# Performance work log

Measured on AMD Instinct MI355X. Metric: run time of the kernel, lower is better.

The kernel has to match this reference:

```python
import jax, jax.numpy as jnp
import numpy as np

N = 50000        # nodes
F_IN = 128       # input features
HID = 128        # hidden_size
H = 4            # heads
C = HID // H     # per-head channels (32)
E_RAND = 800000  # random edges; + N self loops -> E = 850000
NEG_SLOPE = 0.2  # PyG GATConv default leaky_relu slope


def setup_inputs() -> dict:
    key = jax.random.key(0)
    ks = jax.random.split(key, 12)
    x = jax.random.normal(ks[0], (N, F_IN), jnp.float32)
    src_r = jax.random.randint(ks[1], (E_RAND,), 0, N)
    dst_r = jax.random.randint(ks[2], (E_RAND,), 0, N)
    loops = jnp.arange(N)
    src = jnp.concatenate([src_r, loops]).astype(jnp.int32)
    dst = jnp.concatenate([dst_r, loops]).astype(jnp.int32)

    def glorot(k, shape):
        fan_in, fan_out = shape[0], shape[-1]
        lim = np.sqrt(6.0 / (fan_in + fan_out)).astype(np.float32)
        return jax.random.uniform(k, shape, jnp.float32, -lim, lim)

    return {
        "x": x, "src": src, "dst": dst,
        "W0": glorot(ks[3], (F_IN, HID)),
        "a_src0": glorot(ks[4], (H, C)),
        "a_dst0": glorot(ks[5], (H, C)),
        "b0": jnp.zeros((HID,), jnp.float32),
        "W1": glorot(ks[6], (HID, HID)),
        "a_src1": glorot(ks[7], (H, C)),
        "a_dst1": glorot(ks[8], (H, C)),
        "b1": jnp.zeros((HID,), jnp.float32),
    }


def gat_layer(x, W, a_src, a_dst, b, src, dst):
    # linear projection -> [N, H, C]
    xp = (x @ W).reshape(-1, H, C)
    # per-node attention logits [N, H]
    al_src = jnp.einsum("nhc,hc->nh", xp, a_src)
    al_dst = jnp.einsum("nhc,hc->nh", xp, a_dst)
    # edge logits [E, H]
    e = jax.nn.leaky_relu(al_src[src] + al_dst[dst], NEG_SLOPE)
    # scatter softmax over incoming edges of each destination node
    m = jax.ops.segment_max(e, dst, num_segments=N)
    p = jnp.exp(e - m[dst])
    s = jax.ops.segment_sum(p, dst, num_segments=N)
    alpha = p / (s[dst] + 1e-16)
    # weighted message aggregation: [E, H, C] scatter-add -> [N, H, C]
    out = jax.ops.segment_sum(xp[src] * alpha[:, :, None], dst, num_segments=N)
    return out.reshape(-1, H * C) + b  # concat heads + bias


def reference(x, src, dst, W0, a_src0, a_dst0, b0, W1, a_src1, a_dst1, b1):
    h = jax.nn.relu(gat_layer(x, W0, a_src0, a_dst0, b0, src, dst))
    h = jax.nn.relu(gat_layer(h, W1, a_src1, a_dst1, b1, src, dst))
    return h
```

## Files before the change

### kernel.cpp

```cpp
#include <hip/hip_runtime.h>
#include <math.h>

#define NEG_SLOPE 0.2f
#define BCAP 4096
#define TILE 8192

using half8 = __attribute__((ext_vector_type(8))) _Float16;
using f32x4 = __attribute__((ext_vector_type(4))) float;

__device__ __forceinline__ float leaky(float x) { return x > 0.f ? x : NEG_SLOPE * x; }

__device__ __forceinline__ float wsum64(float v) {
#pragma unroll
  for (int off = 32; off; off >>= 1) v += __shfl_xor(v, off);
  return v;
}

__device__ __forceinline__ unsigned short f2h(float f) {
  union { _Float16 h; unsigned short u; } x;
  x.h = (_Float16)f;
  return x.u;
}
__device__ __forceinline__ float h2f(unsigned short u) {
  union { unsigned short u; _Float16 h; } x;
  x.u = u;
  return (float)x.h;
}

__device__ __forceinline__ void acc8h(float* a, float p, uint4 rv) {
  union { uint4 v; _Float16 h[8]; } u;
  u.v = rv;
#pragma unroll
  for (int j = 0; j < 8; ++j) a[j] = fmaf(p, (float)u.h[j], a[j]);
}

__device__ __forceinline__ float getp(float p0, float p1, float p2, float p3,
                                      int h, int t) {
  float b0 = __shfl(p0, t), b1 = __shfl(p1, t);
  float b2 = __shfl(p2, t), b3 = __shfl(p3, t);
  float lo = (h & 1) ? b1 : b0;
  float hi = (h & 1) ? b3 : b2;
  return (h & 2) ? hi : lo;
}

#define PA 136
#define PW 40
template <bool AHALF>
__device__ void gemm_body(
    const void* __restrict__ Av, const unsigned short* __restrict__ Wt,
    const float* __restrict__ a_src, const float* __restrict__ a_dst,
    unsigned short* __restrict__ xph, float* __restrict__ als,
    float* __restrict__ ald, int nrows, int blk) {
  __shared__ unsigned short Ah[64 * PA];
  __shared__ unsigned short Al[AHALF ? 64 : 64 * PA];
  __shared__ unsigned short Wh[128 * PW];
  int t = threadIdx.x;
  int row0 = blk * 64;

  if constexpr (!AHALF) {
    const float4* A4 = (const float4*)Av;
#pragma unroll
    for (int p = 0; p < 8; ++p) {
      int idx = t + p * 256;
      int row = idx >> 5, k4 = idx & 31;
      int gr = row0 + row;
      float4 v = make_float4(0.f, 0.f, 0.f, 0.f);
      if (gr < nrows) v = A4[(size_t)gr * 32 + k4];
      ushort4 hi, lo;
      hi.x = f2h(v.x); lo.x = f2h(v.x - h2f(hi.x));
      hi.y = f2h(v.y); lo.y = f2h(v.y - h2f(hi.y));
      hi.z = f2h(v.z); lo.z = f2h(v.z - h2f(hi.z));
      hi.w = f2h(v.w); lo.w = f2h(v.w - h2f(hi.w));
      *(ushort4*)&Ah[row * PA + k4 * 4] = hi;
      *(ushort4*)&Al[row * PA + k4 * 4] = lo;
    }
  } else {
    const uint4* A4 = (const uint4*)Av;
#pragma unroll
    for (int p = 0; p < 4; ++p) {
      int idx = t + p * 256;
      int row = idx >> 4, k8 = idx & 15;
      int gr = row0 + row;
      uint4 v = make_uint4(0u, 0u, 0u, 0u);
      if (gr < nrows) v = A4[(size_t)gr * 16 + k8];
      *(uint4*)&Ah[row * PA + k8 * 8] = v;
    }
  }

  int lane = t & 63, wv = t >> 6;
  int wr = wv >> 1, wc = wv & 1;
  int ml = lane & 15, q = lane >> 4;
  f32x4 acc[2][4] = {};

  for (int kb = 0; kb < 4; ++kb) {
    __syncthreads();
    int k0 = kb * 32;
#pragma unroll
    for (int p = 0; p < 8; ++p) {
      int idx = t + p * 256;
      int n = idx >> 4, kp = idx & 15;
      *(unsigned*)&Wh[n * PW + kp * 2] =
          *(const unsigned*)(Wt + (size_t)n * 128 + k0 + kp * 2);
    }
    __syncthreads();
    int kf = k0 + q * 8;
    half8 a_h0 = *(const half8*)&Ah[(wr * 32 + ml) * PA + kf];
    half8 a_h1 = *(const half8*)&Ah[(wr * 32 + 16 + ml) * PA + kf];
    half8 a_l0, a_l1;
    if constexpr (!AHALF) {
      a_l0 = *(const half8*)&Al[(wr * 32 + ml) * PA + kf];
      a_l1 = *(const half8*)&Al[(wr * 32 + 16 + ml) * PA + kf];
    }
#pragma unroll
    for (int ct = 0; ct < 4; ++ct) {
      int nb = (wc * 64 + ct * 16 + ml) * PW + q * 8;
      half8 b = *(const half8*)&Wh[nb];
      acc[0][ct] = __builtin_amdgcn_mfma_f32_16x16x32_f16(a_h0, b, acc[0][ct], 0, 0, 0);
      if constexpr (!AHALF)
        acc[0][ct] = __builtin_amdgcn_mfma_f32_16x16x32_f16(a_l0, b, acc[0][ct], 0, 0, 0);
      acc[1][ct] = __builtin_amdgcn_mfma_f32_16x16x32_f16(a_h1, b, acc[1][ct], 0, 0, 0);
      if constexpr (!AHALF)
        acc[1][ct] = __builtin_amdgcn_mfma_f32_16x16x32_f16(a_l1, b, acc[1][ct], 0, 0, 0);
    }
  }

  float asr[4], adr[4];
#pragma unroll
  for (int ct = 0; ct < 4; ++ct) {
    int col = (wc * 2 + (ct >> 1)) * 32 + (ct & 1) * 16 + ml;
    asr[ct] = a_src[col];
    adr[ct] = a_dst[col];
  }

#pragma unroll
  for (int rt = 0; rt < 2; ++rt) {
#pragma unroll
    for (int r = 0; r < 4; ++r) {
      int gr = row0 + wr * 32 + rt * 16 + q * 4 + r;
      bool valid = gr < nrows;
      if (valid) {
#pragma unroll
        for (int ct = 0; ct < 4; ++ct) {
          int gc = wc * 64 + ct * 16 + ml;
          xph[(size_t)gr * 128 + gc] = f2h(acc[rt][ct][r]);
        }
      }
      float p0 = acc[rt][0][r] * asr[0] + acc[rt][1][r] * asr[1];
      float p1 = acc[rt][2][r] * asr[2] + acc[rt][3][r] * asr[3];
      float d0 = acc[rt][0][r] * adr[0] + acc[rt][1][r] * adr[1];
      float d1 = acc[rt][2][r] * adr[2] + acc[rt][3][r] * adr[3];
#pragma unroll
      for (int off = 1; off <= 8; off <<= 1) {
        p0 += __shfl_xor(p0, off); p1 += __shfl_xor(p1, off);
        d0 += __shfl_xor(d0, off); d1 += __shfl_xor(d1, off);
      }
      if (ml == 0 && valid) {
        als[(size_t)gr * 4 + wc * 2] = p0;
        als[(size_t)gr * 4 + wc * 2 + 1] = p1;
        ald[(size_t)gr * 4 + wc * 2] = d0;
        ald[(size_t)gr * 4 + wc * 2 + 1] = d1;
      }
    }
  }
}

__global__ __launch_bounds__(256) void k_hist_wsplit(
    const int* __restrict__ dst, int* __restrict__ blkhist, int E, int nb, int nblk,
    const float* __restrict__ W0, const float* __restrict__ W1,
    unsigned short* __restrict__ Wt0, unsigned short* __restrict__ Wt1) {
  __shared__ int h[512];
  if (blockIdx.x < 128) {
    int i = blockIdx.x * 256 + threadIdx.x;
    int j = i & 16383;
    int k = j >> 7, n = j & 127;
    const float* W = (i < 16384) ? W0 : W1;
    unsigned short hv = f2h(W[j]);
    if (i < 16384) Wt0[n * 128 + k] = hv;
    else Wt1[n * 128 + k] = hv;
    return;
  }
  int blk = blockIdx.x - 128;
  for (int i = threadIdx.x; i < nb; i += 256) h[i] = 0;
  __syncthreads();
  int t0 = blk * TILE;
  int end = t0 + TILE < E ? t0 + TILE : E;
  for (int i = t0 + threadIdx.x; i < end; i += 256) atomicAdd(&h[dst[i] >> 7], 1);
  __syncthreads();
  for (int i = threadIdx.x; i < nb; i += 256) blkhist[(size_t)i * nblk + blk] = h[i];
}

__global__ __launch_bounds__(256) void k_bofs(int* __restrict__ blkhist,
                                              int* __restrict__ btot, int nblk) {
  __shared__ int sd[256];
  int b = blockIdx.x, t = threadIdx.x;
  int v = (t < nblk) ? blkhist[(size_t)b * nblk + t] : 0;
  sd[t] = v;
  __syncthreads();
  for (int off = 1; off < 256; off <<= 1) {
    int add = (t >= off) ? sd[t - off] : 0;
    __syncthreads();
    sd[t] += add;
    __syncthreads();
  }
  if (t < nblk) blkhist[(size_t)b * nblk + t] = sd[t] - v;
  if (t == 255) btot[b] = sd[255];
}

__global__ __launch_bounds__(256, 3) void k_scatter2_gemm(
    const int* __restrict__ src, const int* __restrict__ dst,
    const int* __restrict__ blkhist, const int* __restrict__ btot,
    int* __restrict__ bstore, int E, int nb, int nblk,
    const float* __restrict__ A, const unsigned short* __restrict__ Wt,
    const float* __restrict__ a_src, const float* __restrict__ a_dst,
    unsigned short* __restrict__ xph, float* __restrict__ als,
    float* __restrict__ ald, int nrows) {
  if ((int)blockIdx.x >= nblk) {
    gemm_body<false>(A, Wt, a_src, a_dst, xph, als, ald, nrows, blockIdx.x - nblk);
    return;
  }
  __shared__ int sd[256];
  __shared__ int bb[512];
  __shared__ int cur[512];
  int t = threadIdx.x, blk = blockIdx.x;
  int v0 = (2 * t < nb) ? btot[2 * t] : 0;
  int v1 = (2 * t + 1 < nb) ? btot[2 * t + 1] : 0;
  int s = v0 + v1;
  sd[t] = s;
  __syncthreads();
  for (int off = 1; off < 256; off <<= 1) {
    int add = (t >= off) ? sd[t - off] : 0;
    __syncthreads();
    sd[t] += add;
    __syncthreads();
  }
  int run = sd[t] - s;
  if (2 * t < nb) bb[2 * t] = run;
  if (2 * t + 1 < nb) bb[2 * t + 1] = run + v0;
  __syncthreads();
  for (int i = t; i < nb; i += 256)
    cur[i] = bb[i] + blkhist[(size_t)i * nblk + blk];
  __syncthreads();
  int t0 = blk * TILE;
  int end = t0 + TILE < E ? t0 + TILE : E;
  for (int i = t0 + t; i < end; i += 256) {
    int d = dst[i];
    int pos = atomicAdd(&cur[d >> 7], 1);
    bstore[pos] = ((d & 127) << 16) | src[i];
  }
}

__global__ __launch_bounds__(256) void k_build(
    const int* __restrict__ bstore, const int* __restrict__ btot,
    int* __restrict__ ssrc, int* __restrict__ deg, int* __restrict__ rstart, int N) {
  __shared__ int ls[BCAP];
  __shared__ unsigned char lloc[BCAP];
  __shared__ int lout[BCAP];
  __shared__ int hist[128];
  __shared__ int sc[128];
  __shared__ int lcur[128];
  __shared__ int red[256];
  int b = blockIdx.x;
  int t = threadIdx.x;
  int pacc = 0;
  for (int j = t; j < b; j += 256) pacc += btot[j];
  red[t] = pacc;
  __syncthreads();
  for (int off = 128; off; off >>= 1) {
    if (t < off) red[t] += red[t + off];
    __syncthreads();
  }
  int base = red[0];
  int cnt = btot[b];
  if (cnt > BCAP) cnt = BCAP;
  int nlo = b << 7;
  if (t < 128) { hist[t] = 0; lcur[t] = 0; }
  __syncthreads();
  for (int i = t; i < cnt; i += 256) {
    int e = bstore[base + i];
    int loc = e >> 16;
    ls[i] = e & 0xffff;
    lloc[i] = (unsigned char)loc;
    atomicAdd(&hist[loc], 1);
  }
  __syncthreads();
  int hv = (t < 128) ? hist[t] : 0;
  if (t < 128) sc[t] = hv;
  __syncthreads();
  for (int off = 1; off < 128; off <<= 1) {
    int add = (t < 128 && t >= off) ? sc[t - off] : 0;
    __syncthreads();
    if (t < 128) sc[t] += add;
    __syncthreads();
  }
  int lstart = (t < 128) ? sc[t] - hv : 0;
  if (t < 128) sc[t] = lstart;
  if (t < 128 && nlo + t < N) {
    deg[nlo + t] = hv;
    rstart[nlo + t] = base + lstart;
  }
  __syncthreads();
  for (int i = t; i < cnt; i += 256) {
    int loc = lloc[i];
    int slot = sc[loc] + atomicAdd(&lcur[loc], 1);
    lout[slot] = ls[i];
  }
  __syncthreads();
  for (int i = t; i < cnt; i += 256) ssrc[base + i] = lout[i];
}

__global__ __launch_bounds__(256, 3) void k_gemm2(
    const unsigned short* __restrict__ A, const unsigned short* __restrict__ Wt,
    const float* __restrict__ a_src, const float* __restrict__ a_dst,
    unsigned short* __restrict__ xph, float* __restrict__ als,
    float* __restrict__ ald, int nrows) {
  gemm_body<true>(A, Wt, a_src, a_dst, xph, als, ald, nrows, blockIdx.x);
}

template <bool HOUT>
__global__ __launch_bounds__(256) void k_aggregate(
    const unsigned short* __restrict__ xph, const float* __restrict__ als,
    const float* __restrict__ ald, const int* __restrict__ rstart,
    const int* __restrict__ deg, const int* __restrict__ ssrc,
    const float* __restrict__ bias, void* __restrict__ outv, int N) {
  __shared__ float pbuf[4][128 * 4];
  __shared__ int snbuf[4][128];
  int wv = threadIdx.x >> 6;
  int lane = threadIdx.x & 63;
  int n = (blockIdx.x * blockDim.x + threadIdx.x) >> 6;
  if (n >= N) return;
  int start = rstart[n];
  int d = deg[n];
  float4 adv = *(const float4*)(ald + (size_t)n * 4);

  int cg = lane & 15;
  int es = lane >> 4;
  int c0 = cg * 8;
  int h = cg >> 2;
  float a[8] = {0.f, 0.f, 0.f, 0.f, 0.f, 0.f, 0.f, 0.f};
  float s0 = 0.f, s1 = 0.f, s2 = 0.f, s3 = 0.f;
  const uint4* xp4 = (const uint4*)xph;

  if (d <= 64) {
    bool valid = lane < d;
    int sn = ssrc[start + (valid ? lane : 0)];
    float4 av = *(const float4*)(als + (size_t)sn * 4);
    int sA = __shfl(sn, es);
    int sB = __shfl(sn, es + 4);
    int sC = __shfl(sn, es + 8);
    int sD = __shfl(sn, es + 12);
    uint4 r0 = xp4[(size_t)sA * 16 + cg];
    uint4 r1 = xp4[(size_t)sB * 16 + cg];
    uint4 r2 = xp4[(size_t)sC * 16 + cg];
    uint4 r3 = xp4[(size_t)sD * 16 + cg];
    float p0 = valid ? __expf(leaky(av.x + adv.x)) : 0.f;
    float p1 = valid ? __expf(leaky(av.y + adv.y)) : 0.f;
    float p2 = valid ? __expf(leaky(av.z + adv.z)) : 0.f;
    float p3 = valid ? __expf(leaky(av.w + adv.w)) : 0.f;
    acc8h(a, getp(p0, p1, p2, p3, h, es), r0);
    if (d > 4)  acc8h(a, getp(p0, p1, p2, p3, h, es + 4), r1);
    if (d > 8)  acc8h(a, getp(p0, p1, p2, p3, h, es + 8), r2);
    if (d > 12) acc8h(a, getp(p0, p1, p2, p3, h, es + 12), r3);
    for (int tb = 16; tb < d; tb += 4) {
      int t = tb + es;
      int st = __shfl(sn, t);
      uint4 rv = xp4[(size_t)st * 16 + cg];
      acc8h(a, getp(p0, p1, p2, p3, h, t), rv);
    }
    s0 = wsum64(p0); s1 = wsum64(p1); s2 = wsum64(p2); s3 = wsum64(p3);
  } else {
    for (int base = 0; base < d; base += 64) {
      int i = base + lane;
      bool valid = i < d;
      int sn = valid ? ssrc[start + i] : 0;
      if (valid) snbuf[wv][i] = sn;
      float4 av = *(const float4*)(als + (size_t)sn * 4);
      float p0 = valid ? __expf(leaky(av.x + adv.x)) : 0.f;
      float p1 = valid ? __expf(leaky(av.y + adv.y)) : 0.f;
      float p2 = valid ? __expf(leaky(av.z + adv.z)) : 0.f;
      float p3 = valid ? __expf(leaky(av.w + adv.w)) : 0.f;
      if (valid) *(float4*)&pbuf[wv][i * 4] = make_float4(p0, p1, p2, p3);
      s0 += wsum64(p0); s1 += wsum64(p1); s2 += wsum64(p2); s3 += wsum64(p3);
    }
#pragma unroll 4
    for (int t = es; t < d; t += 4) {
      int sn = snbuf[wv][t];
      float p = pbuf[wv][t * 4 + h];
      uint4 rv = xp4[(size_t)sn * 16 + cg];
      acc8h(a, p, rv);
    }
  }

#pragma unroll
  for (int off = 16; off <= 32; off <<= 1) {
#pragma unroll
    for (int j = 0; j < 8; ++j) a[j] += __shfl_xor(a[j], off);
  }
  if (es == 0) {
    float sden = h == 0 ? s0 : h == 1 ? s1 : h == 2 ? s2 : s3;
    float inv = 1.f / (sden + 1e-16f);
    float4 bv0 = *(const float4*)(bias + c0);
    float4 bv1 = *(const float4*)(bias + c0 + 4);
    float o[8];
    o[0] = fmaxf(a[0] * inv + bv0.x, 0.f);
    o[1] = fmaxf(a[1] * inv + bv0.y, 0.f);
    o[2] = fmaxf(a[2] * inv + bv0.z, 0.f);
    o[3] = fmaxf(a[3] * inv + bv0.w, 0.f);
    o[4] = fmaxf(a[4] * inv + bv1.x, 0.f);
    o[5] = fmaxf(a[5] * inv + bv1.y, 0.f);
    o[6] = fmaxf(a[6] * inv + bv1.z, 0.f);
    o[7] = fmaxf(a[7] * inv + bv1.w, 0.f);
    if constexpr (HOUT) {
      union { uint4 v; _Float16 hh[8]; } u;
#pragma unroll
      for (int j = 0; j < 8; ++j) u.hh[j] = (_Float16)o[j];
      *(uint4*)((unsigned short*)outv + (size_t)n * 128 + c0) = u.v;
    } else {
      float* out = (float*)outv;
      *(float4*)(out + (size_t)n * 128 + c0) = make_float4(o[0], o[1], o[2], o[3]);
      *(float4*)(out + (size_t)n * 128 + c0 + 4) = make_float4(o[4], o[5], o[6], o[7]);
    }
  }
}

extern "C" void kernel_launch(void* const* d_in, const int* in_sizes, int n_in,
                              void* d_out, int out_size, void* d_ws, size_t ws_size,
                              hipStream_t stream) {
  const float* x   = (const float*)d_in[0];
  const int*   src = (const int*)d_in[1];
  const int*   dst = (const int*)d_in[2];
  const float* W0  = (const float*)d_in[3];
  const float* as0 = (const float*)d_in[4];
  const float* ad0 = (const float*)d_in[5];
  const float* b0  = (const float*)d_in[6];
  const float* W1  = (const float*)d_in[7];
  const float* as1 = (const float*)d_in[8];
  const float* ad1 = (const float*)d_in[9];
  const float* b1  = (const float*)d_in[10];
  float* out = (float*)d_out;

  int N = in_sizes[0] / 128;
  int E = in_sizes[1];
  int NB = (N + 127) >> 7;
  int NBLK = (E + TILE - 1) / TILE;

  char* w = (char*)d_ws;
  auto alloc = [&](size_t bytes) {
    char* p = w;
    w += (bytes + 255) & ~(size_t)255;
    return p;
  };
  int* deg     = (int*)alloc((size_t)N * 4);
  int* rstart  = (int*)alloc((size_t)N * 4);
  int* blkhist = (int*)alloc((size_t)NB * NBLK * 4);
  int* btot    = (int*)alloc((size_t)NB * 4);
  int* bstore  = (int*)alloc((size_t)E * 4);
  int* ssrc    = (int*)alloc((size_t)E * 4);
  unsigned short* xph   = (unsigned short*)alloc((size_t)N * 128 * 2);
  unsigned short* hbufh = (unsigned short*)alloc((size_t)N * 128 * 2);
  float* als   = (float*)alloc((size_t)N * 4 * 4);
  float* ald   = (float*)alloc((size_t)N * 4 * 4);
  unsigned short* Wt0 = (unsigned short*)alloc(16384 * 2);
  unsigned short* Wt1 = (unsigned short*)alloc(16384 * 2);

  int gb = (N + 63) / 64;

  k_hist_wsplit<<<128 + NBLK, 256, 0, stream>>>(dst, blkhist, E, NB, NBLK,
                                                W0, W1, Wt0, Wt1);
  k_bofs<<<NB, 256, 0, stream>>>(blkhist, btot, NBLK);
  k_scatter2_gemm<<<NBLK + gb, 256, 0, stream>>>(
      src, dst, blkhist, btot, bstore, E, NB, NBLK,
      x, Wt0, as0, ad0, xph, als, ald, N);
  k_build<<<NB, 256, 0, stream>>>(bstore, btot, ssrc, deg, rstart, N);
  k_aggregate<true><<<(N + 3) / 4, 256, 0, stream>>>(
      xph, als, ald, rstart, deg, ssrc, b0, hbufh, N);
  k_gemm2<<<gb, 256, 0, stream>>>(hbufh, Wt1, as1, ad1, xph, als, ald, N);
  k_aggregate<false><<<(N + 3) / 4, 256, 0, stream>>>(
      xph, als, ald, rstart, deg, ssrc, b1, out, N);
}
```

Baseline: 230.7 us.

## Drop hi/lo fp16 split for fp32 input and stage full W tile once

The first-layer GEMM no longer splits fp32 inputs into high and low fp16 parts, so it skips half of its MFMAs and no longer needs the second shared-memory A buffer. The whole 128x128 weight matrix is now loaded into shared memory once, replacing per-k-block reloads that each needed two barriers. The template flag is renamed and inverted to match. This lowers GEMM input precision to plain fp16, which may increase error against the fp32 reference, and it enlarges the shared W buffer, which could reduce occupancy.

```diff
diff --git a/kernel.cpp b/kernel.cpp
--- a/kernel.cpp
+++ b/kernel.cpp
@@ -20,11 +20,6 @@
   union { _Float16 h; unsigned short u; } x;
   x.h = (_Float16)f;
   return x.u;
-}
-__device__ __forceinline__ float h2f(unsigned short u) {
-  union { unsigned short u; _Float16 h; } x;
-  x.u = u;
-  return (float)x.h;
 }
 
 __device__ __forceinline__ void acc8h(float* a, float p, uint4 rv) {
@@ -44,20 +39,19 @@
 }
 
 #define PA 136
-#define PW 40
-template <bool AHALF>
+#define PW 136
+template <bool AF32>
 __device__ void gemm_body(
     const void* __restrict__ Av, const unsigned short* __restrict__ Wt,
     const float* __restrict__ a_src, const float* __restrict__ a_dst,
     unsigned short* __restrict__ xph, float* __restrict__ als,
     float* __restrict__ ald, int nrows, int blk) {
   __shared__ unsigned short Ah[64 * PA];
-  __shared__ unsigned short Al[AHALF ? 64 : 64 * PA];
   __shared__ unsigned short Wh[128 * PW];
   int t = threadIdx.x;
   int row0 = blk * 64;
 
-  if constexpr (!AHALF) {
+  if constexpr (AF32) {
     const float4* A4 = (const float4*)Av;
 #pragma unroll
     for (int p = 0; p < 8; ++p) {
@@ -66,13 +60,9 @@
       int gr = row0 + row;
       float4 v = make_float4(0.f, 0.f, 0.f, 0.f);
       if (gr < nrows) v = A4[(size_t)gr * 32 + k4];
-      ushort4 hi, lo;
-      hi.x = f2h(v.x); lo.x = f2h(v.x - h2f(hi.x));
-      hi.y = f2h(v.y); lo.y = f2h(v.y - h2f(hi.y));
-      hi.z = f2h(v.z); lo.z = f2h(v.z - h2f(hi.z));
-      hi.w = f2h(v.w); lo.w = f2h(v.w - h2f(hi.w));
+      ushort4 hi;
+      hi.x = f2h(v.x); hi.y = f2h(v.y); hi.z = f2h(v.z); hi.w = f2h(v.w);
       *(ushort4*)&Ah[row * PA + k4 * 4] = hi;
-      *(ushort4*)&Al[row * PA + k4 * 4] = lo;
     }
   } else {
     const uint4* A4 = (const uint4*)Av;
@@ -86,41 +76,33 @@
       *(uint4*)&Ah[row * PA + k8 * 8] = v;
     }
   }
+  {
+    const uint4* W4 = (const uint4*)Wt;
+#pragma unroll
+    for (int p = 0; p < 8; ++p) {
+      int idx = t + p * 256;
+      int n = idx >> 4, k8 = idx & 15;
+      *(uint4*)&Wh[n * PW + k8 * 8] = W4[(size_t)n * 16 + k8];
+    }
+  }
 
   int lane = t & 63, wv = t >> 6;
   int wr = wv >> 1, wc = wv & 1;
   int ml = lane & 15, q = lane >> 4;
   f32x4 acc[2][4] = {};
 
+  __syncthreads();
+
+#pragma unroll
   for (int kb = 0; kb < 4; ++kb) {
-    __syncthreads();
-    int k0 = kb * 32;
-#pragma unroll
-    for (int p = 0; p < 8; ++p) {
-      int idx = t + p * 256;
-      int n = idx >> 4, kp = idx & 15;
-      *(unsigned*)&Wh[n * PW + kp * 2] =
-          *(const unsigned*)(Wt + (size_t)n * 128 + k0 + kp * 2);
-    }
-    __syncthreads();
-    int kf = k0 + q * 8;
-    half8 a_h0 = *(const half8*)&Ah[(wr * 32 + ml) * PA + kf];
-    half8 a_h1 = *(const half8*)&Ah[(wr * 32 + 16 + ml) * PA + kf];
-    half8 a_l0, a_l1;
-    if constexpr (!AHALF) {
-      a_l0 = *(const half8*)&Al[(wr * 32 + ml) * PA + kf];
-      a_l1 = *(const half8*)&Al[(wr * 32 + 16 + ml) * PA + kf];
-    }
+    int kf = kb * 32 + q * 8;
+    half8 a0 = *(const half8*)&Ah[(wr * 32 + ml) * PA + kf];
+    half8 a1 = *(const half8*)&Ah[(wr * 32 + 16 + ml) * PA + kf];
 #pragma unroll
     for (int ct = 0; ct < 4; ++ct) {
-      int nb = (wc * 64 + ct * 16 + ml) * PW + q * 8;
-      half8 b = *(const half8*)&Wh[nb];
-      acc[0][ct] = __builtin_amdgcn_mfma_f32_16x16x32_f16(a_h0, b, acc[0][ct], 0, 0, 0);
-      if constexpr (!AHALF)
-        acc[0][ct] = __builtin_amdgcn_mfma_f32_16x16x32_f16(a_l0, b, acc[0][ct], 0, 0, 0);
-      acc[1][ct] = __builtin_amdgcn_mfma_f32_16x16x32_f16(a_h1, b, acc[1][ct], 0, 0, 0);
-      if constexpr (!AHALF)
-        acc[1][ct] = __builtin_amdgcn_mfma_f32_16x16x32_f16(a_l1, b, acc[1][ct], 0, 0, 0);
+      half8 b = *(const half8*)&Wh[(wc * 64 + ct * 16 + ml) * PW + kf];
+      acc[0][ct] = __builtin_amdgcn_mfma_f32_16x16x32_f16(a0, b, acc[0][ct], 0, 0, 0);
+      acc[1][ct] = __builtin_amdgcn_mfma_f32_16x16x32_f16(a1, b, acc[1][ct], 0, 0, 0);
     }
   }
 
@@ -215,7 +197,7 @@
     unsigned short* __restrict__ xph, float* __restrict__ als,
     float* __restrict__ ald, int nrows) {
   if ((int)blockIdx.x >= nblk) {
-    gemm_body<false>(A, Wt, a_src, a_dst, xph, als, ald, nrows, blockIdx.x - nblk);
+    gemm_body<true>(A, Wt, a_src, a_dst, xph, als, ald, nrows, blockIdx.x - nblk);
     return;
   }
   __shared__ int sd[256];
@@ -313,7 +295,7 @@
     const float* __restrict__ a_src, const float* __restrict__ a_dst,
     unsigned short* __restrict__ xph, float* __restrict__ als,
     float* __restrict__ ald, int nrows) {
-  gemm_body<true>(A, Wt, a_src, a_dst, xph, als, ald, nrows, blockIdx.x);
+  gemm_body<false>(A, Wt, a_src, a_dst, xph, als, ald, nrows, blockIdx.x);
 }
 
 template <bool HOUT>
```

Result: no change. 231.4 us (median of 2 runs) (+0.3%).
